# Kernel tuning notes

Measured on AMD Instinct MI355X. Metric: run time of the kernel, lower is better.

The kernel has to match this reference:

```python
import jax, jax.numpy as jnp
import numpy as np

K, N, E, D = 4, 2048, 4096, 128
BETA = 0.6
EPS = 0.01           # epsilon in hard-sigmoid gating
LAM = 0.05           # lambda_schedule
TC0, TCMAX = 0.3, 0.7
COS_EPS = 1e-8       # F.cosine_similarity eps
MAX_SCORED_EDGES = 500
EDGE_DENSITY = 0.008


def setup_inputs() -> dict:
    key = jax.random.key(0)
    ks = jax.random.split(key, 8)
    s = 0.02
    H = (jax.random.uniform(ks[0], (K, N, E)) < EDGE_DENSITY).astype(jnp.float32)
    X = jax.random.normal(ks[1], (N, D), jnp.float32)
    return dict(
        H=H, X=X, epoch=50,
        mlp_w1=jax.random.normal(ks[2], (K, D, D), jnp.float32) * s,
        mlp_b1=jnp.zeros((K, D), jnp.float32),
        mlp_w2=jax.random.normal(ks[3], (K, D, D), jnp.float32) * s,
        mlp_b2=jnp.zeros((K, D), jnp.float32),
        comp_W=jax.random.normal(ks[4], (K, D, D), jnp.float32) * 0.01,
        att_w1=jax.random.normal(ks[5], (K, D, D // 2), jnp.float32) * s,
        att_b1=jnp.zeros((K, D // 2), jnp.float32),
        att_w2=jax.random.normal(ks[6], (K, D // 2, 1), jnp.float32) * s,
        att_b2=jnp.zeros((K, 1), jnp.float32),
    )


def reference(H, X, epoch, mlp_w1, mlp_b1, mlp_w2, mlp_b2, comp_W,
              att_w1, att_b1, att_w2, att_b2):
    # ---- component level (Eq. 4, batched over K) ----
    h1 = jax.nn.relu(jnp.einsum('nd,kdh->knh', X, mlp_w1) + mlp_b1[:, None, :])
    Xk = jnp.einsum('knh,khe->kne', h1, mlp_w2) + mlp_b2[:, None, :]        # [K,N,D]
    a1 = jax.nn.relu(jnp.einsum('knd,kdh->knh', Xk, att_w1) + att_b1[:, None, :])
    att = jax.nn.sigmoid(jnp.einsum('knh,kho->kno', a1, att_w2) + att_b2[:, None, :])
    S_att = att.mean(axis=(1, 2))                                            # [K]
    frob = jnp.sqrt((comp_W ** 2).sum(axis=(1, 2)))                          # ||W_k||_F
    featn = jnp.sqrt((Xk ** 2).sum(axis=(1, 2)))                             # ||MLP(X_k)||_2 (Frobenius)
    imp = BETA * frob * featn + (1.0 - BETA) * S_att
    pi_c = jax.nn.softmax(imp)
    theta_c = TC0 + (1.0 - jnp.exp(-LAM * epoch)) * (TCMAX - TC0)            # Eq. 3 schedule
    gates = jnp.clip((pi_c - theta_c) / EPS + 0.5, 0.0, 1.0)                 # hard sigmoid
    # K_min = max(1, int(0.1*K)) = 1 -> force top-1 gate open
    keep = jax.nn.one_hot(jnp.argmax(gates), K, dtype=gates.dtype)
    gates = jnp.maximum(gates, keep)

    xnorm = jnp.linalg.norm(X, axis=1)                                       # [N]
    xhat = X / jnp.maximum(xnorm, COS_EPS)[:, None]
    er = jnp.arange(E)
    eye = jnp.eye(N, dtype=bool)

    Hp_l, eg_l, npi_l = [], [], []
    for k in range(K):  # small fixed component count
        Hk = H[k]
        mask = Hk > 0                                                        # [N,E]
        cnt = mask.sum(axis=0)                                               # nodes per hyperedge
        order = jnp.cumsum(mask, axis=0)
        i = jnp.argmax(mask, axis=0)                                         # first incident node
        j = jnp.argmax(mask & (order == 2), axis=0)                          # second incident node
        cos = (xhat[i] * xhat[j]).sum(-1)                                    # [E]
        A = Hk[i, er] * Hk[j, er]                                            # A_ij per edge
        # torch loop: only first 500 edges scored; <2-node edges get 0.1; rest 0
        imp_e = jnp.where(er < MAX_SCORED_EDGES,
                          jnp.where(cnt >= 2, A * cos, 0.1), 0.0)
        pi_e = jax.nn.softmax(imp_e)
        theta_e = jnp.minimum(theta_c, pi_e.mean() + jnp.std(pi_e, ddof=1))  # torch.std unbiased
        eg = jnp.clip((pi_e - theta_e) / EPS + 0.5, 0.0, 1.0)
        eg = jnp.where((eg.sum() < 1.0) & (er == jnp.argmax(pi_e)), 1.0, eg)
        eg_eff = jnp.where(gates[k] > 0.5, eg, jnp.ones_like(eg))
        Hp = Hk * gates[k] * eg_eff[None, :]                                 # pruned incidence

        # ---- node level (Eq. 7) on pruned graph ----
        B = (Hp > 0).astype(Hk.dtype)
        Adj = ((B @ B.T) > 0) & (~eye)                                       # shared-hyperedge neighbors
        degf = Adj.sum(axis=1).astype(Hk.dtype)
        nsum = Adj.astype(Hk.dtype) @ xhat                                   # sum of neighbor unit vecs
        avg = jnp.where(degf > 0, (xhat * nsum).sum(-1) / jnp.maximum(degf, 1.0), 0.0)
        npi = jax.nn.softmax(avg * xnorm)
        Hp_l.append(Hp); eg_l.append(eg); npi_l.append(npi)

    return (jnp.stack(Hp_l), gates, jnp.stack(eg_l), jnp.stack(npi_l))
```

## Files before the change

kernel.cpp:

```cpp
#include <hip/hip_runtime.h>
#include <math.h>

#define KCOMP 4
#define NN 2048
#define EE 4096
#define DD 128
#define MAXNE 96
#define MAXSE 500
#define BETA_C 0.6f
#define EPS_G 0.01f
#define LAM_S 0.05f
#define TC0_C 0.3f
#define TCMAX_C 0.7f
#define COS_EPS_C 1e-8f

typedef float vf4 __attribute__((ext_vector_type(4)));

static const size_t OFF_XHAT   = 0;
static const size_t OFF_XNORM  = 1048576;
static const size_t OFF_SCAL   = 1056768;
static const size_t OFF_NCNT   = 1057024;
static const size_t OFF_EMASK  = 1089792;
static const size_t OFF_NELIST = 5284096;
static const size_t OFF_IMPE   = 6856960;
static const size_t OFF_EGS    = 6865152;
static const size_t OFF_Z      = 6930688;
static const size_t OFF_FEAT   = 6963456;
static const size_t OFF_ATT    = 6965504;
static const size_t OFF_FROB   = 6967552;

__global__ __launch_bounds__(1024) void k_d1(
    const float4* __restrict__ H4, unsigned* __restrict__ emask,
    const float* __restrict__ X, float* __restrict__ xhat, float* __restrict__ xnorm,
    const float* __restrict__ w1, const float* __restrict__ b1,
    const float* __restrict__ w2, const float* __restrict__ b2,
    const float* __restrict__ aw1, const float* __restrict__ ab1,
    const float* __restrict__ aw2, const float* __restrict__ ab2,
    const float4* __restrict__ compW4, int* __restrict__ ncnt,
    unsigned short* __restrict__ nelist,
    float* __restrict__ featA, float* __restrict__ attA, float* __restrict__ frobA) {
  __shared__ float smem[8224];
  int b = blockIdx.x, t = threadIdx.x;
  if (b < 256) {
    int k = b >> 6;
    int bx = b & 63;
    float* Xs  = smem;
    float* H1s = smem + 4096;
    float* A1s = H1s;
    float* red = smem + 8192;
    int n0 = bx * 32;
    for (int i = t; i < 32 * 128; i += 1024) Xs[i] = X[(size_t)n0 * 128 + i];
    __syncthreads();

    int h = t & 127, g = t >> 7;
    const float* W1 = w1 + (size_t)k * 128 * 128;
    float acc[4];
    {
      float bb = b1[k * 128 + h];
#pragma unroll
      for (int rr = 0; rr < 4; ++rr) acc[rr] = bb;
    }
    for (int d = 0; d < 128; d += 4) {
      float wa = W1[(d + 0) * 128 + h];
      float wb = W1[(d + 1) * 128 + h];
      float wc = W1[(d + 2) * 128 + h];
      float wd2 = W1[(d + 3) * 128 + h];
#pragma unroll
      for (int rr = 0; rr < 4; ++rr) {
        float4 x = *(const float4*)&Xs[(g * 4 + rr) * 128 + d];
        acc[rr] = fmaf(x.x, wa, acc[rr]); acc[rr] = fmaf(x.y, wb, acc[rr]);
        acc[rr] = fmaf(x.z, wc, acc[rr]); acc[rr] = fmaf(x.w, wd2, acc[rr]);
      }
    }
#pragma unroll
    for (int rr = 0; rr < 4; ++rr) H1s[(g * 4 + rr) * 128 + h] = fmaxf(acc[rr], 0.f);
    __syncthreads();

    const float* W2 = w2 + (size_t)k * 128 * 128;
    {
      float bb = b2[k * 128 + h];
#pragma unroll
      for (int rr = 0; rr < 4; ++rr) acc[rr] = bb;
    }
    for (int d = 0; d < 128; d += 4) {
      float wa = W2[(d + 0) * 128 + h];
      float wb = W2[(d + 1) * 128 + h];
      float wc = W2[(d + 2) * 128 + h];
      float wd2 = W2[(d + 3) * 128 + h];
#pragma unroll
      for (int rr = 0; rr < 4; ++rr) {
        float4 x = *(const float4*)&H1s[(g * 4 + rr) * 128 + d];
        acc[rr] = fmaf(x.x, wa, acc[rr]); acc[rr] = fmaf(x.y, wb, acc[rr]);
        acc[rr] = fmaf(x.z, wc, acc[rr]); acc[rr] = fmaf(x.w, wd2, acc[rr]);
      }
    }
    float fpart = 0.f;
    __syncthreads();
#pragma unroll
    for (int rr = 0; rr < 4; ++rr) {
      Xs[(g * 4 + rr) * 128 + h] = acc[rr];
      fpart = fmaf(acc[rr], acc[rr], fpart);
    }
    __syncthreads();

    int h2 = t & 63, g4 = t >> 6;
    const float* AW1 = aw1 + (size_t)k * 128 * 64;
    float a2[2];
    {
      float ab = ab1[k * 64 + h2];
      a2[0] = ab; a2[1] = ab;
    }
    for (int d = 0; d < 128; d += 4) {
      float wa = AW1[(d + 0) * 64 + h2];
      float wb = AW1[(d + 1) * 64 + h2];
      float wc = AW1[(d + 2) * 64 + h2];
      float wd2 = AW1[(d + 3) * 64 + h2];
#pragma unroll
      for (int q = 0; q < 2; ++q) {
        float4 x = *(const float4*)&Xs[(g4 * 2 + q) * 128 + d];
        a2[q] = fmaf(x.x, wa, a2[q]); a2[q] = fmaf(x.y, wb, a2[q]);
        a2[q] = fmaf(x.z, wc, a2[q]); a2[q] = fmaf(x.w, wd2, a2[q]);
      }
    }
    __syncthreads();
#pragma unroll
    for (int q = 0; q < 2; ++q) A1s[(g4 * 2 + q) * 64 + h2] = fmaxf(a2[q], 0.f);
    __syncthreads();

    float attsum = 0.f;
    if (t < 32) {
      const float* AW2 = aw2 + (size_t)k * 64;
      float a = ab2[k];
      for (int d = 0; d < 64; d += 4) {
        float4 av = *(const float4*)&A1s[t * 64 + d];
        a = fmaf(av.x, AW2[d + 0], a);
        a = fmaf(av.y, AW2[d + 1], a);
        a = fmaf(av.z, AW2[d + 2], a);
        a = fmaf(av.w, AW2[d + 3], a);
      }
      attsum = 1.f / (1.f + expf(-a));
    }
    for (int o = 32; o > 0; o >>= 1) {
      fpart  += __shfl_xor(fpart, o, 64);
      attsum += __shfl_xor(attsum, o, 64);
    }
    int wv = t >> 6, ln = t & 63;
    if (ln == 0) { red[wv] = fpart; red[16 + wv] = attsum; }
    __syncthreads();
    if (t == 0) {
      float fs = 0.f, as = 0.f;
#pragma unroll
      for (int i = 0; i < 16; i++) { fs += red[i]; as += red[16 + i]; }
      featA[k * 128 + bx] = fs;
      attA[k * 128 + bx]  = as;
    }
    return;
  }
  if (b < 512) {
    unsigned* lds = (unsigned*)smem;
    int sb = b - 256;
    int k = sb >> 6;
    int rem = sb & 63;
    int ch_super = rem >> 4;
    int e4_super = rem & 15;
    int chi = t >> 6;
    int e4i = t & 63;
    int ch = ch_super * 16 + chi;
    int e4 = e4_super * 64 + e4i;
    int n0 = ch * 32;
    const float4* p = H4 + ((size_t)(k * NN + n0)) * (EE / 4) + e4;
    unsigned w0 = 0, w1b = 0, w2b = 0, w3 = 0;
    for (int rb = 0; rb < 32; rb += 8) {
      float4 v[8];
#pragma unroll
      for (int u = 0; u < 8; ++u) v[u] = p[(size_t)(rb + u) * (EE / 4)];
#pragma unroll
      for (int u = 0; u < 8; ++u) {
        unsigned bit = 1u << (rb + u);
        w0  |= (v[u].x > 0.f) ? bit : 0u;
        w1b |= (v[u].y > 0.f) ? bit : 0u;
        w2b |= (v[u].z > 0.f) ? bit : 0u;
        w3  |= (v[u].w > 0.f) ? bit : 0u;
      }
    }
    int el = e4i * 4;
    lds[(el + 0) * 17 + chi] = w0;
    lds[(el + 1) * 17 + chi] = w1b;
    lds[(el + 2) * 17 + chi] = w2b;
    lds[(el + 3) * 17 + chi] = w3;
    {
      int ebase = e4 * 4;
      unsigned ws[4] = {w0, w1b, w2b, w3};
#pragma unroll
      for (int j = 0; j < 4; ++j) {
        unsigned wd = ws[j];
        while (wd) {
          int bit = __builtin_ctz(wd); wd &= wd - 1;
          int node = n0 + bit;
          int slot = atomicAdd(&ncnt[k * NN + node], 1);
          if (slot < MAXNE)
            nelist[((size_t)(k * NN + node)) * MAXNE + slot] =
                (unsigned short)(ebase + j);
        }
      }
    }
    __syncthreads();
    int e_base = e4_super * 256;
    int wi = t & 15;
    int eo = t >> 4;
#pragma unroll
    for (int it = 0; it < 4; ++it) {
      int e_local = it * 64 + eo;
      emask[((size_t)(k * EE) + e_base + e_local) * 64 + ch_super * 16 + wi] =
          lds[e_local * 17 + wi];
    }
    return;
  }
  if (b < 640) {
    int xb = b - 512;
    int node = xb * 16 + (t >> 6);
    int lane = t & 63;
    float2 v = ((const float2*)X)[(size_t)node * 64 + lane];
    float ss = v.x * v.x + v.y * v.y;
    for (int o = 32; o > 0; o >>= 1) ss += __shfl_xor(ss, o, 64);
    float nrm = sqrtf(ss);
    float den = fmaxf(nrm, COS_EPS_C);
    if (lane == 0) xnorm[node] = nrm;
    float2 o2; o2.x = v.x / den; o2.y = v.y / den;
    ((float2*)xhat)[(size_t)node * 64 + lane] = o2;
    return;
  }
  {
    int fb = b - 640;
    int k = fb >> 2, idx = fb & 3;
    float* red = smem;
    float4 v = compW4[(size_t)k * 4096 + idx * 1024 + t];
    float s = v.x * v.x + v.y * v.y + v.z * v.z + v.w * v.w;
    for (int o = 32; o > 0; o >>= 1) s += __shfl_xor(s, o, 64);
    int wv = t >> 6, ln = t & 63;
    if (ln == 0) red[wv] = s;
    __syncthreads();
    if (t == 0) {
      float fs = 0.f;
#pragma unroll
      for (int i = 0; i < 16; i++) fs += red[i];
      frobA[k * 4 + idx] = fs;
    }
  }
}

__global__ void k_d2(const unsigned* __restrict__ emask, const float* __restrict__ xhat,
                     float* __restrict__ impE) {
  int t = threadIdx.x;
  int k = blockIdx.y;
  int bx = blockIdx.x;
  int e = bx * 4 + (t >> 6);
  int lane = t & 63;
  unsigned w = emask[((size_t)(k * EE) + e) * 64 + lane];
  int pc = __popc(w);
  for (int o = 32; o > 0; o >>= 1) pc += __shfl_xor(pc, o, 64);
  float impv = 0.1f;
  if (pc >= 2) {
    unsigned l1 = w ? (unsigned)((lane << 5) + __builtin_ctz(w)) : 0xffffffffu;
    unsigned wr = w & (w - 1);
    unsigned l2 = wr ? (unsigned)((lane << 5) + __builtin_ctz(wr)) : 0xffffffffu;
    unsigned g1 = l1;
    for (int o = 32; o > 0; o >>= 1) {
      unsigned x = (unsigned)__shfl_xor((int)g1, o, 64);
      g1 = g1 < x ? g1 : x;
    }
    unsigned cand = (l1 == g1) ? l2 : l1;
    unsigned g2 = cand;
    for (int o = 32; o > 0; o >>= 1) {
      unsigned x = (unsigned)__shfl_xor((int)g2, o, 64);
      g2 = g2 < x ? g2 : x;
    }
    float2 xi = ((const float2*)xhat)[(size_t)g1 * 64 + lane];
    float2 xj = ((const float2*)xhat)[(size_t)g2 * 64 + lane];
    float d = xi.x * xj.x + xi.y * xj.y;
    for (int o = 32; o > 0; o >>= 1) d += __shfl_xor(d, o, 64);
    impv = d;
  }
  if (lane == 0) impE[k * 512 + e] = impv;
}

__device__ __forceinline__ float blockReduceSum16(float v, float* red, int t) {
  for (int o = 32; o > 0; o >>= 1) v += __shfl_xor(v, o, 64);
  __syncthreads();
  if ((t & 63) == 0) red[t >> 6] = v;
  __syncthreads();
  float s = red[0];
#pragma unroll
  for (int i = 1; i < 16; i++) s += red[i];
  return s;
}

__global__ void k_edgegate(const float* __restrict__ impE,
                           const float* __restrict__ featA, const float* __restrict__ attA,
                           const float* __restrict__ frobA, float* __restrict__ scal,
                           const int* __restrict__ epoch, float* __restrict__ out_gates,
                           float* __restrict__ egscaled, float* __restrict__ out_eg) {
  __shared__ float red[16];
  __shared__ int redi[16];
  __shared__ float imps[KCOMP];
  int k = blockIdx.x;
  int t = threadIdx.x;
  int wv0 = t >> 6, ln0 = t & 63;
  if (wv0 < KCOMP) {
    float pf = featA[wv0 * 128 + ln0];
    float pa = attA[wv0 * 128 + ln0];
    float pr = (ln0 < 4) ? frobA[wv0 * 4 + ln0] : 0.f;
    for (int o = 32; o > 0; o >>= 1) {
      pf += __shfl_xor(pf, o, 64);
      pa += __shfl_xor(pa, o, 64);
      pr += __shfl_xor(pr, o, 64);
    }
    if (ln0 == 0)
      imps[wv0] = BETA_C * sqrtf(pr) * sqrtf(pf) + (1.f - BETA_C) * (pa / (float)NN);
  }
  __syncthreads();
  float gates[KCOMP];
  float tc;
  {
    float mx = imps[0];
    for (int kk = 1; kk < KCOMP; kk++) mx = fmaxf(mx, imps[kk]);
    float ex[KCOMP], ssum = 0.f;
    for (int kk = 0; kk < KCOMP; kk++) { ex[kk] = expf(imps[kk] - mx); ssum += ex[kk]; }
    tc = TC0_C + (1.f - expf(-LAM_S * (float)epoch[0])) * (TCMAX_C - TC0_C);
    for (int kk = 0; kk < KCOMP; kk++) {
      float pi = ex[kk] / ssum;
      gates[kk] = fminf(fmaxf((pi - tc) / EPS_G + 0.5f, 0.f), 1.f);
    }
    int am = 0; float bv2 = gates[0];
    for (int kk = 1; kk < KCOMP; kk++) if (gates[kk] > bv2) { bv2 = gates[kk]; am = kk; }
    gates[am] = fmaxf(gates[am], 1.f);
  }
  if (t == 0) {
    scal[12 + k] = gates[k];
    if (k == 0) for (int kk = 0; kk < KCOMP; kk++) out_gates[kk] = gates[kk];
  }
  float imp[4];
#pragma unroll
  for (int j = 0; j < 4; j++) {
    int e = t + j * 1024;
    imp[j] = (e < MAXSE) ? impE[k * 512 + e] : 0.f;
  }
  float m = fmaxf(fmaxf(imp[0], imp[1]), fmaxf(imp[2], imp[3]));
  for (int o = 32; o > 0; o >>= 1) m = fmaxf(m, __shfl_xor(m, o, 64));
  __syncthreads();
  if ((t & 63) == 0) red[t >> 6] = m;
  __syncthreads();
  m = red[0];
#pragma unroll
  for (int i = 1; i < 16; i++) m = fmaxf(m, red[i]);
  float p[4], psum = 0.f;
#pragma unroll
  for (int j = 0; j < 4; j++) { p[j] = expf(imp[j] - m); psum += p[j]; }
  float S = blockReduceSum16(psum, red, t);
  float pi[4], tot = 0.f;
#pragma unroll
  for (int j = 0; j < 4; j++) { pi[j] = p[j] / S; tot += pi[j]; }
  float T = blockReduceSum16(tot, red, t);
  float mean = T / (float)EE;
  float devs = 0.f;
#pragma unroll
  for (int j = 0; j < 4; j++) { float d = pi[j] - mean; devs = fmaf(d, d, devs); }
  float V = blockReduceSum16(devs, red, t);
  float stdv = sqrtf(V / (float)(EE - 1));
  float theta = fminf(tc, mean + stdv);
  float eg[4], egsum = 0.f;
#pragma unroll
  for (int j = 0; j < 4; j++) {
    eg[j] = fminf(fmaxf((pi[j] - theta) / EPS_G + 0.5f, 0.f), 1.f);
    egsum += eg[j];
  }
  float EGS = blockReduceSum16(egsum, red, t);
  float bv = -1e30f; int bi = 0x7fffffff;
#pragma unroll
  for (int j = 0; j < 4; j++) if (pi[j] > bv) { bv = pi[j]; bi = t + j * 1024; }
  for (int o = 32; o > 0; o >>= 1) {
    float ov = __shfl_xor(bv, o, 64); int oi = __shfl_xor(bi, o, 64);
    if (ov > bv || (ov == bv && oi < bi)) { bv = ov; bi = oi; }
  }
  __syncthreads();
  if ((t & 63) == 0) { red[t >> 6] = bv; redi[t >> 6] = bi; }
  __syncthreads();
  float abv = red[0]; int abi = redi[0];
#pragma unroll
  for (int i = 1; i < 16; i++) {
    float ov = red[i]; int oi = redi[i];
    if (ov > abv || (ov == abv && oi < abi)) { abv = ov; abi = oi; }
  }
  float g = gates[k];
#pragma unroll
  for (int j = 0; j < 4; j++) {
    int e = t + j * 1024;
    float egv = eg[j];
    if (EGS < 1.f && e == abi) egv = 1.f;
    out_eg[(size_t)k * EE + e] = egv;
    float eff = (g > 0.5f) ? egv : 1.f;
    egscaled[k * EE + e] = g * eff;
  }
}

__global__ void k_hprow(const unsigned* __restrict__ emask,
                        const int* __restrict__ ncnt, const unsigned short* __restrict__ nelist,
                        const float* __restrict__ egs, const float* __restrict__ scal,
                        const float* __restrict__ xhat, const float* __restrict__ xnorm,
                        float* __restrict__ out, float* __restrict__ z) {
  __shared__ float row[EE];
  __shared__ unsigned short elds[MAXNE];
  __shared__ unsigned wpart[4][64];
  __shared__ unsigned short list[2048];
  __shared__ int cnt_s;
  __shared__ float sred[4];
  int k = blockIdx.y, n = blockIdx.x, t = threadIdx.x;
  float g = scal[12 + k];
  vf4* o4 = (vf4*)(out + ((size_t)(k * NN + n)) * EE);
  if (g <= 0.f) {
    vf4 z4 = {0.f, 0.f, 0.f, 0.f};
#pragma unroll
    for (int i = 0; i < 4; i++) __builtin_nontemporal_store(z4, &o4[t + i * 256]);
    if (t == 0) z[k * NN + n] = 0.f;
    return;
  }
  int ec = ncnt[k * NN + n]; if (ec > MAXNE) ec = MAXNE;
  if (t < ec) elds[t] = nelist[((size_t)(k * NN + n)) * MAXNE + t];
  vf4* row4 = (vf4*)row;
  vf4 z4 = {0.f, 0.f, 0.f, 0.f};
#pragma unroll
  for (int i = 0; i < 4; i++) row4[t + i * 256] = z4;
  if (t == 0) cnt_s = 0;
  __syncthreads();
  if (t < ec) {
    int e = elds[t];
    row[e] = egs[k * EE + e];
  }
  __syncthreads();
#pragma unroll
  for (int i = 0; i < 4; i++) __builtin_nontemporal_store(row4[t + i * 256], &o4[t + i * 256]);
  int lane = t & 63, wv = t >> 6;
  unsigned acc = 0;
  for (int it = wv; it < ec; it += 4) {
    int e = (int)elds[it];
    if (row[e] > 0.f) acc |= emask[((size_t)(k * EE) + e) * 64 + lane];
  }
  wpart[wv][lane] = acc;
  __syncthreads();
  if (t < 64) {
    unsigned w = wpart[0][t] | wpart[1][t] | wpart[2][t] | wpart[3][t];
    if (t == (n >> 5)) w &= ~(1u << (n & 31));
    int c = __popc(w);
    if (c > 0) {
      int base = atomicAdd(&cnt_s, c);
      while (w) {
        int b = __builtin_ctz(w); w &= w - 1;
        list[base++] = (unsigned short)((t << 5) + b);
      }
    }
  }
  __syncthreads();
  int cnt = cnt_s;
  if (cnt == 0) { if (t == 0) z[k * NN + n] = 0.f; return; }
  int fc = lane & 31, hh = lane >> 5;
  float4 xn4 = ((const float4*)xhat)[(size_t)n * 32 + fc];
  float a = 0.f;
#pragma unroll 4
  for (int it = wv * 2 + hh; it < cnt; it += 8) {
    int m = (int)list[it];
    float4 xm = ((const float4*)xhat)[(size_t)m * 32 + fc];
    a += xn4.x * xm.x + xn4.y * xm.y + xn4.z * xm.z + xn4.w * xm.w;
  }
  for (int o = 32; o > 0; o >>= 1) a += __shfl_xor(a, o, 64);
  if (lane == 0) sred[wv] = a;
  __syncthreads();
  if (t == 0) {
    float s = sred[0] + sred[1] + sred[2] + sred[3];
    z[k * NN + n] = (s / (float)cnt) * xnorm[n];
  }
}

__global__ void k_npi(const float* __restrict__ z, float* __restrict__ out_npi) {
  __shared__ float red[4];
  int k = blockIdx.x, t = threadIdx.x;
  float v[8]; float m = -1e30f;
#pragma unroll
  for (int j = 0; j < 8; j++) { v[j] = z[k * NN + t + j * 256]; m = fmaxf(m, v[j]); }
  for (int o = 32; o > 0; o >>= 1) m = fmaxf(m, __shfl_xor(m, o, 64));
  if ((t & 63) == 0) red[t >> 6] = m;
  __syncthreads();
  m = fmaxf(fmaxf(red[0], red[1]), fmaxf(red[2], red[3]));
  __syncthreads();
  float pe[8]; float s = 0.f;
#pragma unroll
  for (int j = 0; j < 8; j++) { pe[j] = expf(v[j] - m); s += pe[j]; }
  for (int o = 32; o > 0; o >>= 1) s += __shfl_xor(s, o, 64);
  if ((t & 63) == 0) red[t >> 6] = s;
  __syncthreads();
  s = red[0] + red[1] + red[2] + red[3];
#pragma unroll
  for (int j = 0; j < 8; j++) out_npi[k * NN + t + j * 256] = pe[j] / s;
}

extern "C" void kernel_launch(void* const* d_in, const int* in_sizes, int n_in,
                              void* d_out, int out_size, void* d_ws, size_t ws_size,
                              hipStream_t stream) {
  const float* H     = (const float*)d_in[0];
  const float* X     = (const float*)d_in[1];
  const int*   epoch = (const int*)d_in[2];
  const float* w1    = (const float*)d_in[3];
  const float* b1    = (const float*)d_in[4];
  const float* w2    = (const float*)d_in[5];
  const float* b2    = (const float*)d_in[6];
  const float* compW = (const float*)d_in[7];
  const float* aw1   = (const float*)d_in[8];
  const float* ab1   = (const float*)d_in[9];
  const float* aw2   = (const float*)d_in[10];
  const float* ab2   = (const float*)d_in[11];

  char* ws = (char*)d_ws;
  float* xhat  = (float*)(ws + OFF_XHAT);
  float* xnorm = (float*)(ws + OFF_XNORM);
  float* scal  = (float*)(ws + OFF_SCAL);
  int*   ncnt  = (int*)(ws + OFF_NCNT);
  unsigned* emask = (unsigned*)(ws + OFF_EMASK);
  unsigned short* nelist = (unsigned short*)(ws + OFF_NELIST);
  float* impE  = (float*)(ws + OFF_IMPE);
  float* egs   = (float*)(ws + OFF_EGS);
  float* zbuf  = (float*)(ws + OFF_Z);
  float* featA = (float*)(ws + OFF_FEAT);
  float* attA  = (float*)(ws + OFF_ATT);
  float* frobA = (float*)(ws + OFF_FROB);

  float* out       = (float*)d_out;
  float* out_gates = out + (size_t)KCOMP * NN * EE;
  float* out_eg    = out_gates + KCOMP;
  float* out_npi   = out_eg + (size_t)KCOMP * EE;

  hipMemsetAsync(ncnt, 0, (size_t)KCOMP * NN * sizeof(int), stream);
  k_d1<<<656, 1024, 0, stream>>>((const float4*)H, emask, X, xhat, xnorm,
                                 w1, b1, w2, b2, aw1, ab1, aw2, ab2,
                                 (const float4*)compW, ncnt, nelist, featA, attA, frobA);
  k_d2<<<dim3(125, KCOMP), 256, 0, stream>>>(emask, xhat, impE);
  k_edgegate<<<KCOMP, 1024, 0, stream>>>(impE, featA, attA, frobA, scal, epoch,
                                         out_gates, egs, out_eg);
  k_hprow<<<dim3(NN, KCOMP), 256, 0, stream>>>(emask, ncnt, nelist, egs, scal, xhat, xnorm,
                                               out, zbuf);
  k_npi<<<KCOMP, 256, 0, stream>>>(zbuf, out_npi);
}
```

Baseline: 303.6 us.

## Split fused prologue kernel into three and drop LDS row staging in k_hprow

The multi-role k_d1 kernel is split into k_scan (incidence bitmask and node-edge lists), k_mlp (MLP/attention features) and k_xfr (normalized X and comp_W Frobenius). Each kernel gets its own LDS size and register allocation instead of the worst case of all roles, at the price of extra launches that now run one after another. k_hprow no longer zeroes a 16 KB LDS row and copies it out. It streams zeros straight to the output row, then scatters the few nonzero gate values after a barrier, which removes LDS traffic and raises occupancy. The scatter depends on global-memory ordering between the zero stores and the later stores from the same block.

```diff
diff --git a/kernel.cpp b/kernel.cpp
--- a/kernel.cpp
+++ b/kernel.cpp
@@ -29,196 +29,198 @@
 static const size_t OFF_ATT    = 6965504;
 static const size_t OFF_FROB   = 6967552;
 
-__global__ __launch_bounds__(1024) void k_d1(
+__global__ __launch_bounds__(1024) void k_scan(
     const float4* __restrict__ H4, unsigned* __restrict__ emask,
-    const float* __restrict__ X, float* __restrict__ xhat, float* __restrict__ xnorm,
+    int* __restrict__ ncnt, unsigned short* __restrict__ nelist) {
+  __shared__ unsigned lds[256 * 17];
+  int sb = blockIdx.x, t = threadIdx.x;
+  int k = sb >> 6;
+  int rem = sb & 63;
+  int ch_super = rem >> 4;
+  int e4_super = rem & 15;
+  int chi = t >> 6;
+  int e4i = t & 63;
+  int ch = ch_super * 16 + chi;
+  int e4 = e4_super * 64 + e4i;
+  int n0 = ch * 32;
+  const float4* p = H4 + ((size_t)(k * NN + n0)) * (EE / 4) + e4;
+  unsigned w0 = 0, w1b = 0, w2b = 0, w3 = 0;
+  for (int rb = 0; rb < 32; rb += 8) {
+    float4 v[8];
+#pragma unroll
+    for (int u = 0; u < 8; ++u) v[u] = p[(size_t)(rb + u) * (EE / 4)];
+#pragma unroll
+    for (int u = 0; u < 8; ++u) {
+      unsigned bit = 1u << (rb + u);
+      w0  |= (v[u].x > 0.f) ? bit : 0u;
+      w1b |= (v[u].y > 0.f) ? bit : 0u;
+      w2b |= (v[u].z > 0.f) ? bit : 0u;
+      w3  |= (v[u].w > 0.f) ? bit : 0u;
+    }
+  }
+  int el = e4i * 4;
+  lds[(el + 0) * 17 + chi] = w0;
+  lds[(el + 1) * 17 + chi] = w1b;
+  lds[(el + 2) * 17 + chi] = w2b;
+  lds[(el + 3) * 17 + chi] = w3;
+  {
+    int ebase = e4 * 4;
+    unsigned ws[4] = {w0, w1b, w2b, w3};
+#pragma unroll
+    for (int j = 0; j < 4; ++j) {
+      unsigned wd = ws[j];
+      while (wd) {
+        int bit = __builtin_ctz(wd); wd &= wd - 1;
+        int node = n0 + bit;
+        int slot = atomicAdd(&ncnt[k * NN + node], 1);
+        if (slot < MAXNE)
+          nelist[((size_t)(k * NN + node)) * MAXNE + slot] =
+              (unsigned short)(ebase + j);
+      }
+    }
+  }
+  __syncthreads();
+  int e_base = e4_super * 256;
+  int wi = t & 15;
+  int eo = t >> 4;
+#pragma unroll
+  for (int it = 0; it < 4; ++it) {
+    int e_local = it * 64 + eo;
+    emask[((size_t)(k * EE) + e_base + e_local) * 64 + ch_super * 16 + wi] =
+        lds[e_local * 17 + wi];
+  }
+}
+
+__global__ __launch_bounds__(1024) void k_mlp(
+    const float* __restrict__ X,
     const float* __restrict__ w1, const float* __restrict__ b1,
     const float* __restrict__ w2, const float* __restrict__ b2,
     const float* __restrict__ aw1, const float* __restrict__ ab1,
     const float* __restrict__ aw2, const float* __restrict__ ab2,
-    const float4* __restrict__ compW4, int* __restrict__ ncnt,
-    unsigned short* __restrict__ nelist,
-    float* __restrict__ featA, float* __restrict__ attA, float* __restrict__ frobA) {
+    float* __restrict__ featA, float* __restrict__ attA) {
   __shared__ float smem[8224];
   int b = blockIdx.x, t = threadIdx.x;
-  if (b < 256) {
-    int k = b >> 6;
-    int bx = b & 63;
-    float* Xs  = smem;
-    float* H1s = smem + 4096;
-    float* A1s = H1s;
-    float* red = smem + 8192;
-    int n0 = bx * 32;
-    for (int i = t; i < 32 * 128; i += 1024) Xs[i] = X[(size_t)n0 * 128 + i];
-    __syncthreads();
-
-    int h = t & 127, g = t >> 7;
-    const float* W1 = w1 + (size_t)k * 128 * 128;
-    float acc[4];
-    {
-      float bb = b1[k * 128 + h];
-#pragma unroll
-      for (int rr = 0; rr < 4; ++rr) acc[rr] = bb;
-    }
-    for (int d = 0; d < 128; d += 4) {
-      float wa = W1[(d + 0) * 128 + h];
-      float wb = W1[(d + 1) * 128 + h];
-      float wc = W1[(d + 2) * 128 + h];
-      float wd2 = W1[(d + 3) * 128 + h];
-#pragma unroll
-      for (int rr = 0; rr < 4; ++rr) {
-        float4 x = *(const float4*)&Xs[(g * 4 + rr) * 128 + d];
-        acc[rr] = fmaf(x.x, wa, acc[rr]); acc[rr] = fmaf(x.y, wb, acc[rr]);
-        acc[rr] = fmaf(x.z, wc, acc[rr]); acc[rr] = fmaf(x.w, wd2, acc[rr]);
-      }
-    }
-#pragma unroll
-    for (int rr = 0; rr < 4; ++rr) H1s[(g * 4 + rr) * 128 + h] = fmaxf(acc[rr], 0.f);
-    __syncthreads();
-
-    const float* W2 = w2 + (size_t)k * 128 * 128;
-    {
-      float bb = b2[k * 128 + h];
-#pragma unroll
-      for (int rr = 0; rr < 4; ++rr) acc[rr] = bb;
-    }
-    for (int d = 0; d < 128; d += 4) {
-      float wa = W2[(d + 0) * 128 + h];
-      float wb = W2[(d + 1) * 128 + h];
-      float wc = W2[(d + 2) * 128 + h];
-      float wd2 = W2[(d + 3) * 128 + h];
-#pragma unroll
-      for (int rr = 0; rr < 4; ++rr) {
-        float4 x = *(const float4*)&H1s[(g * 4 + rr) * 128 + d];
-        acc[rr] = fmaf(x.x, wa, acc[rr]); acc[rr] = fmaf(x.y, wb, acc[rr]);
-        acc[rr] = fmaf(x.z, wc, acc[rr]); acc[rr] = fmaf(x.w, wd2, acc[rr]);
-      }
-    }
-    float fpart = 0.f;
-    __syncthreads();
+  int k = b >> 6;
+  int bx = b & 63;
+  float* Xs  = smem;
+  float* H1s = smem + 4096;
+  float* A1s = H1s;
+  float* red = smem + 8192;
+  int n0 = bx * 32;
+  for (int i = t; i < 32 * 128; i += 1024) Xs[i] = X[(size_t)n0 * 128 + i];
+  __syncthreads();
+
+  int h = t & 127, g = t >> 7;
+  const float* W1 = w1 + (size_t)k * 128 * 128;
+  float acc[4];
+  {
+    float bb = b1[k * 128 + h];
+#pragma unroll
+    for (int rr = 0; rr < 4; ++rr) acc[rr] = bb;
+  }
+  for (int d = 0; d < 128; d += 4) {
+    float wa = W1[(d + 0) * 128 + h];
+    float wb = W1[(d + 1) * 128 + h];
+    float wc = W1[(d + 2) * 128 + h];
+    float wd2 = W1[(d + 3) * 128 + h];
 #pragma unroll
     for (int rr = 0; rr < 4; ++rr) {
-      Xs[(g * 4 + rr) * 128 + h] = acc[rr];
-      fpart = fmaf(acc[rr], acc[rr], fpart);
-    }
-    __syncthreads();
-
-    int h2 = t & 63, g4 = t >> 6;
-    const float* AW1 = aw1 + (size_t)k * 128 * 64;
-    float a2[2];
-    {
-      float ab = ab1[k * 64 + h2];
-      a2[0] = ab; a2[1] = ab;
-    }
-    for (int d = 0; d < 128; d += 4) {
-      float wa = AW1[(d + 0) * 64 + h2];
-      float wb = AW1[(d + 1) * 64 + h2];
-      float wc = AW1[(d + 2) * 64 + h2];
-      float wd2 = AW1[(d + 3) * 64 + h2];
-#pragma unroll
-      for (int q = 0; q < 2; ++q) {
-        float4 x = *(const float4*)&Xs[(g4 * 2 + q) * 128 + d];
-        a2[q] = fmaf(x.x, wa, a2[q]); a2[q] = fmaf(x.y, wb, a2[q]);
-        a2[q] = fmaf(x.z, wc, a2[q]); a2[q] = fmaf(x.w, wd2, a2[q]);
-      }
-    }
-    __syncthreads();
-#pragma unroll
-    for (int q = 0; q < 2; ++q) A1s[(g4 * 2 + q) * 64 + h2] = fmaxf(a2[q], 0.f);
-    __syncthreads();
-
-    float attsum = 0.f;
-    if (t < 32) {
-      const float* AW2 = aw2 + (size_t)k * 64;
-      float a = ab2[k];
-      for (int d = 0; d < 64; d += 4) {
-        float4 av = *(const float4*)&A1s[t * 64 + d];
-        a = fmaf(av.x, AW2[d + 0], a);
-        a = fmaf(av.y, AW2[d + 1], a);
-        a = fmaf(av.z, AW2[d + 2], a);
-        a = fmaf(av.w, AW2[d + 3], a);
-      }
-      attsum = 1.f / (1.f + expf(-a));
-    }
-    for (int o = 32; o > 0; o >>= 1) {
-      fpart  += __shfl_xor(fpart, o, 64);
-      attsum += __shfl_xor(attsum, o, 64);
-    }
-    int wv = t >> 6, ln = t & 63;
-    if (ln == 0) { red[wv] = fpart; red[16 + wv] = attsum; }
-    __syncthreads();
-    if (t == 0) {
-      float fs = 0.f, as = 0.f;
-#pragma unroll
-      for (int i = 0; i < 16; i++) { fs += red[i]; as += red[16 + i]; }
-      featA[k * 128 + bx] = fs;
-      attA[k * 128 + bx]  = as;
-    }
-    return;
-  }
-  if (b < 512) {
-    unsigned* lds = (unsigned*)smem;
-    int sb = b - 256;
-    int k = sb >> 6;
-    int rem = sb & 63;
-    int ch_super = rem >> 4;
-    int e4_super = rem & 15;
-    int chi = t >> 6;
-    int e4i = t & 63;
-    int ch = ch_super * 16 + chi;
-    int e4 = e4_super * 64 + e4i;
-    int n0 = ch * 32;
-    const float4* p = H4 + ((size_t)(k * NN + n0)) * (EE / 4) + e4;
-    unsigned w0 = 0, w1b = 0, w2b = 0, w3 = 0;
-    for (int rb = 0; rb < 32; rb += 8) {
-      float4 v[8];
-#pragma unroll
-      for (int u = 0; u < 8; ++u) v[u] = p[(size_t)(rb + u) * (EE / 4)];
-#pragma unroll
-      for (int u = 0; u < 8; ++u) {
-        unsigned bit = 1u << (rb + u);
-        w0  |= (v[u].x > 0.f) ? bit : 0u;
-        w1b |= (v[u].y > 0.f) ? bit : 0u;
-        w2b |= (v[u].z > 0.f) ? bit : 0u;
-        w3  |= (v[u].w > 0.f) ? bit : 0u;
-      }
-    }
-    int el = e4i * 4;
-    lds[(el + 0) * 17 + chi] = w0;
-    lds[(el + 1) * 17 + chi] = w1b;
-    lds[(el + 2) * 17 + chi] = w2b;
-    lds[(el + 3) * 17 + chi] = w3;
-    {
-      int ebase = e4 * 4;
-      unsigned ws[4] = {w0, w1b, w2b, w3};
-#pragma unroll
-      for (int j = 0; j < 4; ++j) {
-        unsigned wd = ws[j];
-        while (wd) {
-          int bit = __builtin_ctz(wd); wd &= wd - 1;
-          int node = n0 + bit;
-          int slot = atomicAdd(&ncnt[k * NN + node], 1);
-          if (slot < MAXNE)
-            nelist[((size_t)(k * NN + node)) * MAXNE + slot] =
-                (unsigned short)(ebase + j);
-        }
-      }
-    }
-    __syncthreads();
-    int e_base = e4_super * 256;
-    int wi = t & 15;
-    int eo = t >> 4;
-#pragma unroll
-    for (int it = 0; it < 4; ++it) {
-      int e_local = it * 64 + eo;
-      emask[((size_t)(k * EE) + e_base + e_local) * 64 + ch_super * 16 + wi] =
-          lds[e_local * 17 + wi];
-    }
-    return;
-  }
-  if (b < 640) {
-    int xb = b - 512;
-    int node = xb * 16 + (t >> 6);
+      float4 x = *(const float4*)&Xs[(g * 4 + rr) * 128 + d];
+      acc[rr] = fmaf(x.x, wa, acc[rr]); acc[rr] = fmaf(x.y, wb, acc[rr]);
+      acc[rr] = fmaf(x.z, wc, acc[rr]); acc[rr] = fmaf(x.w, wd2, acc[rr]);
+    }
+  }
+#pragma unroll
+  for (int rr = 0; rr < 4; ++rr) H1s[(g * 4 + rr) * 128 + h] = fmaxf(acc[rr], 0.f);
+  __syncthreads();
+
+  const float* W2 = w2 + (size_t)k * 128 * 128;
+  {
+    float bb = b2[k * 128 + h];
+#pragma unroll
+    for (int rr = 0; rr < 4; ++rr) acc[rr] = bb;
+  }
+  for (int d = 0; d < 128; d += 4) {
+    float wa = W2[(d + 0) * 128 + h];
+    float wb = W2[(d + 1) * 128 + h];
+    float wc = W2[(d + 2) * 128 + h];
+    float wd2 = W2[(d + 3) * 128 + h];
+#pragma unroll
+    for (int rr = 0; rr < 4; ++rr) {
+      float4 x = *(const float4*)&H1s[(g * 4 + rr) * 128 + d];
+      acc[rr] = fmaf(x.x, wa, acc[rr]); acc[rr] = fmaf(x.y, wb, acc[rr]);
+      acc[rr] = fmaf(x.z, wc, acc[rr]); acc[rr] = fmaf(x.w, wd2, acc[rr]);
+    }
+  }
+  float fpart = 0.f;
+  __syncthreads();
+#pragma unroll
+  for (int rr = 0; rr < 4; ++rr) {
+    Xs[(g * 4 + rr) * 128 + h] = acc[rr];
+    fpart = fmaf(acc[rr], acc[rr], fpart);
+  }
+  __syncthreads();
+
+  int h2 = t & 63, g4 = t >> 6;
+  const float* AW1 = aw1 + (size_t)k * 128 * 64;
+  float a2[2];
+  {
+    float ab = ab1[k * 64 + h2];
+    a2[0] = ab; a2[1] = ab;
+  }
+  for (int d = 0; d < 128; d += 4) {
+    float wa = AW1[(d + 0) * 64 + h2];
+    float wb = AW1[(d + 1) * 64 + h2];
+    float wc = AW1[(d + 2) * 64 + h2];
+    float wd2 = AW1[(d + 3) * 64 + h2];
+#pragma unroll
+    for (int q = 0; q < 2; ++q) {
+      float4 x = *(const float4*)&Xs[(g4 * 2 + q) * 128 + d];
+      a2[q] = fmaf(x.x, wa, a2[q]); a2[q] = fmaf(x.y, wb, a2[q]);
+      a2[q] = fmaf(x.z, wc, a2[q]); a2[q] = fmaf(x.w, wd2, a2[q]);
+    }
+  }
+  __syncthreads();
+#pragma unroll
+  for (int q = 0; q < 2; ++q) A1s[(g4 * 2 + q) * 64 + h2] = fmaxf(a2[q], 0.f);
+  __syncthreads();
+
+  float attsum = 0.f;
+  if (t < 32) {
+    const float* AW2 = aw2 + (size_t)k * 64;
+    float a = ab2[k];
+    for (int d = 0; d < 64; d += 4) {
+      float4 av = *(const float4*)&A1s[t * 64 + d];
+      a = fmaf(av.x, AW2[d + 0], a);
+      a = fmaf(av.y, AW2[d + 1], a);
+      a = fmaf(av.z, AW2[d + 2], a);
+      a = fmaf(av.w, AW2[d + 3], a);
+    }
+    attsum = 1.f / (1.f + expf(-a));
+  }
+  for (int o = 32; o > 0; o >>= 1) {
+    fpart  += __shfl_xor(fpart, o, 64);
+    attsum += __shfl_xor(attsum, o, 64);
+  }
+  int wv = t >> 6, ln = t & 63;
+  if (ln == 0) { red[wv] = fpart; red[16 + wv] = attsum; }
+  __syncthreads();
+  if (t == 0) {
+    float fs = 0.f, as = 0.f;
+#pragma unroll
+    for (int i = 0; i < 16; i++) { fs += red[i]; as += red[16 + i]; }
+    featA[k * 128 + bx] = fs;
+    attA[k * 128 + bx]  = as;
+  }
+}
+
+__global__ __launch_bounds__(1024) void k_xfr(
+    const float* __restrict__ X, float* __restrict__ xhat, float* __restrict__ xnorm,
+    const float4* __restrict__ compW4, float* __restrict__ frobA) {
+  __shared__ float red[16];
+  int b = blockIdx.x, t = threadIdx.x;
+  if (b < 128) {
+    int node = b * 16 + (t >> 6);
     int lane = t & 63;
     float2 v = ((const float2*)X)[(size_t)node * 64 + lane];
     float ss = v.x * v.x + v.y * v.y;
@@ -230,22 +232,19 @@
     ((float2*)xhat)[(size_t)node * 64 + lane] = o2;
     return;
   }
-  {
-    int fb = b - 640;
-    int k = fb >> 2, idx = fb & 3;
-    float* red = smem;
-    float4 v = compW4[(size_t)k * 4096 + idx * 1024 + t];
-    float s = v.x * v.x + v.y * v.y + v.z * v.z + v.w * v.w;
-    for (int o = 32; o > 0; o >>= 1) s += __shfl_xor(s, o, 64);
-    int wv = t >> 6, ln = t & 63;
-    if (ln == 0) red[wv] = s;
-    __syncthreads();
-    if (t == 0) {
-      float fs = 0.f;
-#pragma unroll
-      for (int i = 0; i < 16; i++) fs += red[i];
-      frobA[k * 4 + idx] = fs;
-    }
+  int fb = b - 128;
+  int k = fb >> 2, idx = fb & 3;
+  float4 v = compW4[(size_t)k * 4096 + idx * 1024 + t];
+  float s = v.x * v.x + v.y * v.y + v.z * v.z + v.w * v.w;
+  for (int o = 32; o > 0; o >>= 1) s += __shfl_xor(s, o, 64);
+  int wv = t >> 6, ln = t & 63;
+  if (ln == 0) red[wv] = s;
+  __syncthreads();
+  if (t == 0) {
+    float fs = 0.f;
+#pragma unroll
+    for (int i = 0; i < 16; i++) fs += red[i];
+    frobA[k * 4 + idx] = fs;
   }
 }
 
@@ -408,42 +407,38 @@
                         const float* __restrict__ egs, const float* __restrict__ scal,
                         const float* __restrict__ xhat, const float* __restrict__ xnorm,
                         float* __restrict__ out, float* __restrict__ z) {
-  __shared__ float row[EE];
   __shared__ unsigned short elds[MAXNE];
+  __shared__ float evals[MAXNE];
   __shared__ unsigned wpart[4][64];
   __shared__ unsigned short list[2048];
   __shared__ int cnt_s;
   __shared__ float sred[4];
   int k = blockIdx.y, n = blockIdx.x, t = threadIdx.x;
   float g = scal[12 + k];
-  vf4* o4 = (vf4*)(out + ((size_t)(k * NN + n)) * EE);
+  float* orow = out + ((size_t)(k * NN + n)) * EE;
+  vf4* o4 = (vf4*)orow;
+  vf4 z4 = {0.f, 0.f, 0.f, 0.f};
   if (g <= 0.f) {
-    vf4 z4 = {0.f, 0.f, 0.f, 0.f};
 #pragma unroll
     for (int i = 0; i < 4; i++) __builtin_nontemporal_store(z4, &o4[t + i * 256]);
     if (t == 0) z[k * NN + n] = 0.f;
     return;
   }
   int ec = ncnt[k * NN + n]; if (ec > MAXNE) ec = MAXNE;
-  if (t < ec) elds[t] = nelist[((size_t)(k * NN + n)) * MAXNE + t];
-  vf4* row4 = (vf4*)row;
-  vf4 z4 = {0.f, 0.f, 0.f, 0.f};
-#pragma unroll
-  for (int i = 0; i < 4; i++) row4[t + i * 256] = z4;
   if (t == 0) cnt_s = 0;
-  __syncthreads();
   if (t < ec) {
-    int e = elds[t];
-    row[e] = egs[k * EE + e];
-  }
-  __syncthreads();
-#pragma unroll
-  for (int i = 0; i < 4; i++) __builtin_nontemporal_store(row4[t + i * 256], &o4[t + i * 256]);
+    int e = nelist[((size_t)(k * NN + n)) * MAXNE + t];
+    elds[t] = (unsigned short)e;
+    evals[t] = egs[k * EE + e];
+  }
+#pragma unroll
+  for (int i = 0; i < 4; i++) __builtin_nontemporal_store(z4, &o4[t + i * 256]);
+  __syncthreads();
+  if (t < ec) orow[elds[t]] = evals[t];
   int lane = t & 63, wv = t >> 6;
   unsigned acc = 0;
   for (int it = wv; it < ec; it += 4) {
-    int e = (int)elds[it];
-    if (row[e] > 0.f) acc |= emask[((size_t)(k * EE) + e) * 64 + lane];
+    if (evals[it] > 0.f) acc |= emask[((size_t)(k * EE) + elds[it]) * 64 + lane];
   }
   wpart[wv][lane] = acc;
   __syncthreads();
@@ -538,9 +533,9 @@
   float* out_npi   = out_eg + (size_t)KCOMP * EE;
 
   hipMemsetAsync(ncnt, 0, (size_t)KCOMP * NN * sizeof(int), stream);
-  k_d1<<<656, 1024, 0, stream>>>((const float4*)H, emask, X, xhat, xnorm,
-                                 w1, b1, w2, b2, aw1, ab1, aw2, ab2,
-                                 (const float4*)compW, ncnt, nelist, featA, attA, frobA);
+  k_scan<<<256, 1024, 0, stream>>>((const float4*)H, emask, ncnt, nelist);
+  k_mlp<<<256, 1024, 0, stream>>>(X, w1, b1, w2, b2, aw1, ab1, aw2, ab2, featA, attA);
+  k_xfr<<<144, 1024, 0, stream>>>(X, xhat, xnorm, (const float4*)compW, frobA);
   k_d2<<<dim3(125, KCOMP), 256, 0, stream>>>(emask, xhat, impE);
   k_edgegate<<<KCOMP, 1024, 0, stream>>>(impE, featA, attA, frobA, scal, epoch,
                                          out_gates, egs, out_eg);
```

After: 321.3 us. 1.06x slower.
